# Performance work log

Measured on AMD Instinct MI355X. Metric: run time of the kernel, lower is better.

Reference implementation:

```python
import jax, jax.numpy as jnp
import numpy as np

B = 16          # number of point clouds (equal-sized, contiguous batch ids)
NC_PER = 1024   # coarse points per cloud
NF_PER = 4096   # fine points per cloud
K = 3           # knn_interpolate neighbors
C_IN = 512      # coarse feature channels
C_SKIP = 256    # skip feature channels
C_OUT = 512
BN_EPS = 1e-5


def setup_inputs() -> dict:
    key = jax.random.key(0)
    ks = jax.random.split(key, 8)
    Nc, Nf = B * NC_PER, B * NF_PER
    d_in = C_IN + C_SKIP
    x = jax.random.normal(ks[0], (Nc, C_IN), jnp.float32)
    pos = jax.random.uniform(ks[1], (Nc, 3), jnp.float32)
    batch = jnp.repeat(jnp.arange(B, dtype=jnp.int64), NC_PER)
    x_skip = jax.random.normal(ks[2], (Nf, C_SKIP), jnp.float32)
    pos_skip = jax.random.uniform(ks[3], (Nf, 3), jnp.float32)
    batch_skip = jnp.repeat(jnp.arange(B, dtype=jnp.int64), NF_PER)
    W1 = jax.random.normal(ks[4], (d_in, C_OUT), jnp.float32) / np.sqrt(d_in)
    W2 = jax.random.normal(ks[5], (C_OUT, C_OUT), jnp.float32) / np.sqrt(C_OUT)
    return {
        "x": x, "pos": pos, "batch": batch,
        "x_skip": x_skip, "pos_skip": pos_skip, "batch_skip": batch_skip,
        "W1": W1, "b1": jnp.zeros((C_OUT,), jnp.float32),
        "g1": jnp.ones((C_OUT,), jnp.float32), "be1": jnp.zeros((C_OUT,), jnp.float32),
        "W2": W2, "b2": jnp.zeros((C_OUT,), jnp.float32),
        "g2": jnp.ones((C_OUT,), jnp.float32), "be2": jnp.zeros((C_OUT,), jnp.float32),
    }


def _knn_interpolate(x, pos, pos_skip):
    # batches are contiguous and equal-sized -> reshape to [B, n, .] (honors batch/batch_skip)
    xb = x.reshape(B, NC_PER, C_IN)
    pc = pos.reshape(B, NC_PER, 3)
    pf = pos_skip.reshape(B, NF_PER, 3)
    # squared pairwise distances [B, NF_PER, NC_PER] via ||a||^2 + ||b||^2 - 2ab
    d2 = ((pf * pf).sum(-1)[:, :, None]
          + (pc * pc).sum(-1)[:, None, :]
          - 2.0 * jnp.einsum('bfd,bcd->bfc', pf, pc))
    neg_d2, idx = jax.lax.top_k(-d2, K)           # [B, NF_PER, K]
    w = 1.0 / jnp.maximum(-neg_d2, 1e-16)         # inverse squared-distance weights
    gathered = jax.vmap(lambda xi, ii: xi[ii])(xb, idx)   # [B, NF_PER, K, C_IN]
    y = (w[..., None] * gathered).sum(2) / w.sum(2)[..., None]
    return y.reshape(B * NF_PER, C_IN)


def _bn_act(h, g, be):
    # BatchNorm1d in training mode (biased variance) + ReLU
    mu = h.mean(0)
    var = ((h - mu) ** 2).mean(0)
    return jax.nn.relu((h - mu) * jax.lax.rsqrt(var + BN_EPS) * g + be)


def reference(x, pos, batch, x_skip, pos_skip, batch_skip,
              W1, b1, g1, be1, W2, b2, g2, be2):
    xi = _knn_interpolate(x, pos, pos_skip)        # [Nf, C_IN]
    h = jnp.concatenate([xi, x_skip], axis=1)      # [Nf, C_IN + C_SKIP]
    h = _bn_act(h @ W1 + b1, g1, be1)
    h = _bn_act(h @ W2 + b2, g2, be2)
    return (h, pos_skip, batch_skip)
```

## Files before the change

### kernel.cpp

```cpp
#include <hip/hip_runtime.h>
#include <cstdint>
#include <cstddef>

#define BATCHES   16
#define NC_PER    1024
#define NF_PER    4096
#define NC_TOT    (BATCHES * NC_PER)
#define NF_TOT    (BATCHES * NF_PER)
#define C_IN      512
#define C_SKIP    256
#define D_IN      (C_IN + C_SKIP)
#define C_OUT     512
#define BN_EPS    1e-5f

typedef __bf16 bf16x8 __attribute__((ext_vector_type(8)));
typedef __bf16 bf16x4 __attribute__((ext_vector_type(4)));
typedef float  f32x4  __attribute__((ext_vector_type(4)));

static_assert(sizeof(__bf16) == 2, "bf16 size");

__global__ __launch_bounds__(256) void transpose_to_bf16(
    const float* __restrict__ W, __bf16* __restrict__ Wt, int K, int N) {
  int idx = blockIdx.x * 256 + threadIdx.x;
  if (idx >= K * N) return;
  int n = idx / K;
  int k = idx - n * K;
  Wt[idx] = (__bf16)W[k * N + n];
}

__global__ __launch_bounds__(256) void knn_kernel(
    const float* __restrict__ pos,
    const float* __restrict__ pos_skip,
    int4*  __restrict__ idx3,
    float4* __restrict__ w3)
{
  __shared__ float s_pos[NC_PER * 3];
  __shared__ float s_pc2[NC_PER];
  __shared__ float s_pd[4][64][3];
  __shared__ int   s_pi[4][64][3];

  const int tid   = threadIdx.x;
  const int bi    = blockIdx.x;
  const int fbase = bi * 64;
  const int b     = fbase >> 12;
  const int cbase = b * NC_PER;

  for (int i = tid; i < NC_PER * 3; i += 256)
    s_pos[i] = pos[(size_t)cbase * 3 + i];
  __syncthreads();
  for (int j = tid; j < NC_PER; j += 256) {
    float cx = s_pos[j * 3 + 0], cy = s_pos[j * 3 + 1], cz = s_pos[j * 3 + 2];
    s_pc2[j] = __fadd_rn(__fadd_rn(__fmul_rn(cx, cx), __fmul_rn(cy, cy)),
                         __fmul_rn(cz, cz));
  }
  __syncthreads();

  const int p   = tid & 63;
  const int seg = tid >> 6;
  const int f   = fbase + p;
  const float px = pos_skip[f * 3 + 0];
  const float py = pos_skip[f * 3 + 1];
  const float pz = pos_skip[f * 3 + 2];
  const float pf2 = __fadd_rn(__fadd_rn(__fmul_rn(px, px), __fmul_rn(py, py)),
                              __fmul_rn(pz, pz));
  float b0 = 1e30f, b1 = 1e30f, b2 = 1e30f;
  int   i0 = 0,     i1 = 0,     i2 = 0;
  const int j0 = seg * 256;
#pragma unroll 4
  for (int jj = 0; jj < 256; ++jj) {
    const int j = j0 + jj;
    float cx = s_pos[j * 3 + 0], cy = s_pos[j * 3 + 1], cz = s_pos[j * 3 + 2];
    float dot = __fadd_rn(__fadd_rn(__fmul_rn(px, cx), __fmul_rn(py, cy)),
                          __fmul_rn(pz, cz));
    float d2 = __fsub_rn(__fadd_rn(pf2, s_pc2[j]), __fmul_rn(2.0f, dot));
    if (d2 < b2) {
      if (d2 < b1) {
        b2 = b1; i2 = i1;
        if (d2 < b0) { b1 = b0; i1 = i0; b0 = d2; i0 = j; }
        else         { b1 = d2; i1 = j; }
      } else { b2 = d2; i2 = j; }
    }
  }
  s_pd[seg][p][0] = b0; s_pd[seg][p][1] = b1; s_pd[seg][p][2] = b2;
  s_pi[seg][p][0] = i0; s_pi[seg][p][1] = i1; s_pi[seg][p][2] = i2;
  __syncthreads();

  if (tid < 64) {
    float m0 = 1e30f, m1 = 1e30f, m2 = 1e30f;
    int  mi0 = 0,    mi1 = 0,    mi2 = 0;
#pragma unroll
    for (int s = 0; s < 4; ++s)
#pragma unroll
      for (int k = 0; k < 3; ++k) {
        float d = s_pd[s][tid][k];
        int   i = s_pi[s][tid][k];
        if (d < m2 || (d == m2 && i < mi2)) {
          if (d < m1 || (d == m1 && i < mi1)) {
            m2 = m1; mi2 = mi1;
            if (d < m0 || (d == m0 && i < mi0)) {
              m1 = m0; mi1 = mi0; m0 = d; mi0 = i;
            } else { m1 = d; mi1 = i; }
          } else { m2 = d; mi2 = i; }
        }
      }
    float w0 = 1.0f / fmaxf(m0, 1e-16f);
    float w1 = 1.0f / fmaxf(m1, 1e-16f);
    float w2 = 1.0f / fmaxf(m2, 1e-16f);
    float inv = 1.0f / __fadd_rn(__fadd_rn(w0, w1), w2);
    const int fo = fbase + tid;
    idx3[fo] = make_int4(mi0, mi1, mi2, 0);
    w3[fo]   = make_float4(w0 * inv, w1 * inv, w2 * inv, 0.f);
  }
}

__global__ __launch_bounds__(256) void gather_interp(
    const float* __restrict__ x,
    const float* __restrict__ x_skip,
    const int4*  __restrict__ idx3,
    const float4* __restrict__ w3,
    __bf16* __restrict__ h0)
{
  const int bi   = blockIdx.x;
  const int xcd  = bi & 7;
  const int slot = bi >> 3;
  const int batch = xcd * 2 + (slot >> 10);
  const int blk   = slot & 1023;
  const int wv = threadIdx.x >> 6, ln = threadIdx.x & 63;
  const int f = batch * NF_PER + blk * 4 + wv;
  const int cbase = batch * NC_PER;

  const int4   id = idx3[f];
  const float4 w  = w3[f];
  const float* x0 = x + (size_t)(cbase + id.x) * C_IN;
  const float* x1 = x + (size_t)(cbase + id.y) * C_IN;
  const float* x2 = x + (size_t)(cbase + id.z) * C_IN;
  __bf16* o = h0 + (size_t)f * D_IN;
  const int c0 = ln * 4;
#pragma unroll
  for (int it = 0; it < 2; ++it) {
    const int c = c0 + it * 256;
    float4 a0 = *(const float4*)(x0 + c);
    float4 a1 = *(const float4*)(x1 + c);
    float4 a2 = *(const float4*)(x2 + c);
    bf16x4 ov;
    ov[0] = (__bf16)(w.x * a0.x + w.y * a1.x + w.z * a2.x);
    ov[1] = (__bf16)(w.x * a0.y + w.y * a1.y + w.z * a2.y);
    ov[2] = (__bf16)(w.x * a0.z + w.y * a1.z + w.z * a2.z);
    ov[3] = (__bf16)(w.x * a0.w + w.y * a1.w + w.z * a2.w);
    *(bf16x4*)(o + c) = ov;
  }
  float4 s = *(const float4*)(x_skip + (size_t)f * C_SKIP + c0);
  bf16x4 sv;
  sv[0] = (__bf16)s.x; sv[1] = (__bf16)s.y;
  sv[2] = (__bf16)s.z; sv[3] = (__bf16)s.w;
  *(bf16x4*)(o + C_IN + c0) = sv;
}

template <int K, bool BF16OUT>
__global__ __launch_bounds__(512, 2) void gemm_bt(
    const __bf16* __restrict__ A,
    const __bf16* __restrict__ Bt,
    const float*  __restrict__ bias,
    void* __restrict__ Cout,
    float* __restrict__ part1)
{
  constexpr int NT = K / 64;
  __shared__ __align__(16) __bf16 As[2 * 16384];
  __shared__ __align__(16) __bf16 Bs[2 * 16384];
  __shared__ float s_red[4][4][16][2];

  const int tid  = threadIdx.x;
  const int wave = tid >> 6, lane = tid & 63;
  const int quad = lane >> 4, l16 = lane & 15;
  const int wm = wave >> 2, wn = wave & 3;

  const int bid  = blockIdx.x;
  const int work = (bid & 7) * 64 + (bid >> 3);
  const int mt = work >> 1, nt = work & 1;
  const int m0 = mt * 256, n0 = nt * 256;

  const int rowA = wave * 8 + (lane >> 3);
  const int kOff = ((lane & 7) ^ (lane >> 3)) * 8;
  const int ldsChunkBase = (wave * 64) * 8;

  auto stage_half = [&](const __bf16* __restrict__ src, int rowBase, int t,
                        __bf16* dst) {
#pragma unroll
    for (int q = 0; q < 2; ++q) {
      __builtin_amdgcn_global_load_lds(
          (const __attribute__((address_space(1))) unsigned int*)(
              src + (size_t)(rowBase + q * 64 + rowA) * K + t * 64 + kOff),
          (__attribute__((address_space(3))) unsigned int*)(
              dst + q * 4096 + ldsChunkBase),
          16, 0, 0);
    }
  };

  f32x4 acc[8][4] = {};
  const int swz  = (l16 & 7) << 3;
  const int brow = (wn & 1) * 64;

  stage_half(A,  m0,       0, As);
  stage_half(Bt, n0,       0, Bs);
  stage_half(A,  m0 + 128, 0, As + 8192);
  stage_half(Bt, n0 + 128, 0, Bs + 8192);

  bf16x8 aA[4][2], bB[4][2];
#pragma unroll 2
  for (int t = 0; t < NT; ++t) {
    const int cur = t & 1;
    const __bf16* Ab = As + (cur * 2 + wm) * 8192;
    const __bf16* Bb = Bs + (cur * 2 + (wn >> 1)) * 8192;
    __bf16* Asn = As + (cur ^ 1) * 16384;
    __bf16* Bsn = Bs + (cur ^ 1) * 16384;

    if (t + 1 < NT) {
      stage_half(A,  m0,       t + 1, Asn);
      stage_half(Bt, n0,       t + 1, Bsn);
      asm volatile("s_waitcnt vmcnt(4)" ::: "memory");
    } else {
      asm volatile("s_waitcnt vmcnt(0)" ::: "memory");
    }
    __builtin_amdgcn_sched_barrier(0);
    __builtin_amdgcn_s_barrier();
#pragma unroll
    for (int mf = 0; mf < 4; ++mf)
#pragma unroll
      for (int ks = 0; ks < 2; ++ks)
        aA[mf][ks] = *(const bf16x8*)(Ab + (mf * 16 + l16) * 64 +
                                      ((ks * 32 + quad * 8) ^ swz));
#pragma unroll
    for (int nf = 0; nf < 2; ++nf)
#pragma unroll
      for (int ks = 0; ks < 2; ++ks)
        bB[nf][ks] = *(const bf16x8*)(Bb + (brow + nf * 16 + l16) * 64 +
                                      ((ks * 32 + quad * 8) ^ swz));
    __builtin_amdgcn_s_setprio(1);
#pragma unroll
    for (int mf = 0; mf < 4; ++mf)
#pragma unroll
      for (int nf = 0; nf < 2; ++nf)
#pragma unroll
        for (int ks = 0; ks < 2; ++ks)
          acc[mf][nf] = __builtin_amdgcn_mfma_f32_16x16x32_bf16(
              aA[mf][ks], bB[nf][ks], acc[mf][nf], 0, 0, 0);
    __builtin_amdgcn_s_setprio(0);
    __builtin_amdgcn_s_barrier();

    if (t + 1 < NT) {
      stage_half(A,  m0 + 128, t + 1, Asn + 8192);
      stage_half(Bt, n0 + 128, t + 1, Bsn + 8192);
    }
#pragma unroll
    for (int nf = 2; nf < 4; ++nf)
#pragma unroll
      for (int ks = 0; ks < 2; ++ks)
        bB[nf][ks] = *(const bf16x8*)(Bb + (brow + nf * 16 + l16) * 64 +
                                      ((ks * 32 + quad * 8) ^ swz));
    __builtin_amdgcn_s_setprio(1);
#pragma unroll
    for (int mf = 0; mf < 4; ++mf)
#pragma unroll
      for (int nf = 2; nf < 4; ++nf)
#pragma unroll
        for (int ks = 0; ks < 2; ++ks)
          acc[mf][nf] = __builtin_amdgcn_mfma_f32_16x16x32_bf16(
              aA[mf][ks], bB[nf][ks], acc[mf][nf], 0, 0, 0);
    __builtin_amdgcn_s_setprio(0);
    __builtin_amdgcn_s_barrier();

#pragma unroll
    for (int mf = 0; mf < 4; ++mf)
#pragma unroll
      for (int ks = 0; ks < 2; ++ks)
        aA[mf][ks] = *(const bf16x8*)(Ab + (64 + mf * 16 + l16) * 64 +
                                      ((ks * 32 + quad * 8) ^ swz));
    __builtin_amdgcn_s_setprio(1);
#pragma unroll
    for (int mf = 0; mf < 4; ++mf)
#pragma unroll
      for (int nf = 0; nf < 2; ++nf)
#pragma unroll
        for (int ks = 0; ks < 2; ++ks)
          acc[4 + mf][nf] = __builtin_amdgcn_mfma_f32_16x16x32_bf16(
              aA[mf][ks], bB[nf][ks], acc[4 + mf][nf], 0, 0, 0);
    __builtin_amdgcn_s_setprio(0);
    __builtin_amdgcn_s_barrier();

    __builtin_amdgcn_s_setprio(1);
#pragma unroll
    for (int mf = 0; mf < 4; ++mf)
#pragma unroll
      for (int nf = 2; nf < 4; ++nf)
#pragma unroll
        for (int ks = 0; ks < 2; ++ks)
          acc[4 + mf][nf] = __builtin_amdgcn_mfma_f32_16x16x32_bf16(
              aA[mf][ks], bB[nf][ks], acc[4 + mf][nf], 0, 0, 0);
    __builtin_amdgcn_s_setprio(0);
    __builtin_amdgcn_s_barrier();
  }

  float sArr[4], ssArr[4];
#pragma unroll
  for (int nf = 0; nf < 4; ++nf) {
    const int n = n0 + wn * 64 + nf * 16 + l16;
    const float bv = bias[n];
    float s = 0.f, ss = 0.f;
#pragma unroll
    for (int mf = 0; mf < 8; ++mf) {
      const int mb = m0 + wm * 128 + mf * 16 + quad * 4;
#pragma unroll
      for (int r = 0; r < 4; ++r) {
        const float v = acc[mf][nf][r] + bv;
        s += v; ss += v * v;
        if constexpr (BF16OUT)
          ((__bf16*)Cout)[(size_t)(mb + r) * 512 + n] = (__bf16)v;
        else
          ((float*)Cout)[(size_t)(mb + r) * 512 + n] = v;
      }
    }
    s  += __shfl_down(s, 32);  s  += __shfl_down(s, 16);
    ss += __shfl_down(ss, 32); ss += __shfl_down(ss, 16);
    sArr[nf] = s; ssArr[nf] = ss;
  }
  if (wm == 1 && quad == 0) {
#pragma unroll
    for (int nf = 0; nf < 4; ++nf) {
      s_red[wn][nf][l16][0] = sArr[nf];
      s_red[wn][nf][l16][1] = ssArr[nf];
    }
  }
  asm volatile("s_waitcnt lgkmcnt(0)" ::: "memory");
  __builtin_amdgcn_s_barrier();
  if (wm == 0 && quad == 0) {
    float* row = part1 + (size_t)mt * 1024;
#pragma unroll
    for (int nf = 0; nf < 4; ++nf) {
      const int n = n0 + wn * 64 + nf * 16 + l16;
      row[n]       = sArr[nf]  + s_red[wn][nf][l16][0];
      row[512 + n] = ssArr[nf] + s_red[wn][nf][l16][1];
    }
  }
}

__global__ __launch_bounds__(256) void reduce_partials(
    const float* __restrict__ part1, float* __restrict__ part2) {
  const int rb = blockIdx.x;
  const int t  = threadIdx.x;
#pragma unroll
  for (int k = 0; k < 4; ++k) {
    const int c = k * 256 + t;
    float acc = 0.f;
    const float* p = part1 + (size_t)rb * 16 * 1024 + c;
#pragma unroll
    for (int r = 0; r < 16; ++r) { acc += *p; p += 1024; }
    part2[rb * 1024 + c] = acc;
  }
}

__global__ void finalize_stats(const float* __restrict__ part2,
                               const float* __restrict__ g,
                               const float* __restrict__ be,
                               float* __restrict__ ab, float invM) {
  const int c = blockIdx.x * 256 + threadIdx.x;
  if (c < 512) {
    float s = 0.f, ss = 0.f;
#pragma unroll
    for (int r = 0; r < 16; ++r) {
      s  += part2[r * 1024 + c];
      ss += part2[r * 1024 + 512 + c];
    }
    float mean = s * invM;
    float var  = ss * invM - mean * mean;
    float a = g[c] * rsqrtf(var + BN_EPS);
    ab[c] = a;
    ab[512 + c] = be[c] - mean * a;
  }
}

__global__ __launch_bounds__(256) void bnrelu_bf16(
    __bf16* __restrict__ H, const float* __restrict__ ab) {
  const size_t e = ((size_t)blockIdx.x * 256 + threadIdx.x) * 4;
  const int c = (int)(e & 511);
  bf16x4* p = (bf16x4*)(H + e);
  bf16x4 h = *p;
#pragma unroll
  for (int i = 0; i < 4; ++i) {
    float v = (float)h[i];
    v = fmaxf(fmaf(v, ab[c + i], ab[512 + c + i]), 0.f);
    h[i] = (__bf16)v;
  }
  *p = h;
}

__global__ __launch_bounds__(256) void bnrelu_b2f(
    const __bf16* __restrict__ H, const float* __restrict__ ab,
    float* __restrict__ O) {
  const size_t e = ((size_t)blockIdx.x * 256 + threadIdx.x) * 4;
  const int c = (int)(e & 511);
  bf16x4 h = *(const bf16x4*)(H + e);
  float4 o;
  o.x = fmaxf(fmaf((float)h[0], ab[c + 0], ab[512 + c + 0]), 0.f);
  o.y = fmaxf(fmaf((float)h[1], ab[c + 1], ab[512 + c + 1]), 0.f);
  o.z = fmaxf(fmaf((float)h[2], ab[c + 2], ab[512 + c + 2]), 0.f);
  o.w = fmaxf(fmaf((float)h[3], ab[c + 3], ab[512 + c + 3]), 0.f);
  *(float4*)(O + e) = o;
}

__global__ __launch_bounds__(256) void tail_kernel(
    const float* __restrict__ pos_skip, float* __restrict__ out2) {
  const int i = blockIdx.x * 256 + threadIdx.x;
  if (i < NF_TOT * 3) {
    out2[i] = pos_skip[i];
  } else {
    const int f = i - NF_TOT * 3;
    out2[i] = (float)(f >> 12);
  }
}

extern "C" void kernel_launch(void* const* d_in, const int* in_sizes, int n_in,
                              void* d_out, int out_size, void* d_ws, size_t ws_size,
                              hipStream_t stream) {
  (void)in_sizes; (void)n_in; (void)out_size; (void)ws_size;

  const float* x        = (const float*)d_in[0];
  const float* pos      = (const float*)d_in[1];
  const float* x_skip   = (const float*)d_in[3];
  const float* pos_skip = (const float*)d_in[4];
  const float* W1  = (const float*)d_in[6];
  const float* b1  = (const float*)d_in[7];
  const float* g1  = (const float*)d_in[8];
  const float* be1 = (const float*)d_in[9];
  const float* W2  = (const float*)d_in[10];
  const float* b2  = (const float*)d_in[11];
  const float* g2  = (const float*)d_in[12];
  const float* be2 = (const float*)d_in[13];
  float* out = (float*)d_out;

  char* ws = (char*)d_ws;
  __bf16* h0   = (__bf16*)(ws);
  __bf16* h2   = (__bf16*)(ws);
  __bf16* h1   = (__bf16*)(ws + 100663296ull);
  __bf16* W1t  = (__bf16*)(ws + 167772160ull);
  __bf16* W2t  = (__bf16*)(ws + 168558592ull);
  float*  ab1   = (float*)(ws + 169086976ull);
  float*  ab2   = (float*)(ws + 169095168ull);
  int4*   idx3  = (int4*)(ws + 169099264ull);
  float4* w3    = (float4*)(ws + 170147840ull);
  float*  part1 = (float*)(ws + 169099264ull);
  float*  part2 = (float*)(ws + 171196416ull);

  transpose_to_bf16<<<(D_IN * C_OUT + 255) / 256, 256, 0, stream>>>(W1, W1t, D_IN, C_OUT);
  transpose_to_bf16<<<(C_OUT * C_OUT + 255) / 256, 256, 0, stream>>>(W2, W2t, C_OUT, C_OUT);

  knn_kernel<<<NF_TOT / 64, 256, 0, stream>>>(pos, pos_skip, idx3, w3);
  gather_interp<<<NF_TOT / 4, 256, 0, stream>>>(x, x_skip, idx3, w3, h0);

  gemm_bt<D_IN, true><<<512, 512, 0, stream>>>(h0, W1t, b1, (void*)h1, part1);
  reduce_partials<<<16, 256, 0, stream>>>(part1, part2);
  finalize_stats<<<2, 256, 0, stream>>>(part2, g1, be1, ab1, 1.0f / (float)NF_TOT);
  bnrelu_bf16<<<(NF_TOT * 512 / 4) / 256, 256, 0, stream>>>(h1, ab1);

  gemm_bt<C_OUT, true><<<512, 512, 0, stream>>>(h1, W2t, b2, (void*)h2, part1);
  reduce_partials<<<16, 256, 0, stream>>>(part1, part2);
  finalize_stats<<<2, 256, 0, stream>>>(part2, g2, be2, ab2, 1.0f / (float)NF_TOT);
  bnrelu_b2f<<<(NF_TOT * 512 / 4) / 256, 256, 0, stream>>>(h2, ab2, out);

  tail_kernel<<<(NF_TOT * 3 + NF_TOT + 255) / 256, 256, 0, stream>>>(
      pos_skip, out + (size_t)NF_TOT * 512);
}
```

Before: 506.4 us.

## Fuse BN1+ReLU into second GEMM A-load and stage GEMM output through LDS

Removes the standalone bnrelu_bf16 pass by loading GEMM2's A tiles into registers, applying the BN scale/shift and ReLU, and writing them to LDS inside the pipelined K-loop. The GEMM epilogue now stages bf16 outputs through LDS so that global stores are coalesced 16-byte rows instead of scattered 2-byte writes. It also merges the two weight transposes into one launch and widens bnrelu_b2f to 8 elements per thread. The trade-off is extra VALU work and a register round-trip for A inside GEMM2's main loop, plus more complex wait-count handling.

Result: faster. 472.0 us (-6.8%).

```diff
diff --git a/kernel.cpp b/kernel.cpp
--- a/kernel.cpp
+++ b/kernel.cpp
@@ -19,13 +19,26 @@
 
 static_assert(sizeof(__bf16) == 2, "bf16 size");
 
-__global__ __launch_bounds__(256) void transpose_to_bf16(
-    const float* __restrict__ W, __bf16* __restrict__ Wt, int K, int N) {
+__device__ __forceinline__ bf16x8 load16(const __bf16* p) {
+  f32x4 r;
+  asm volatile("global_load_dwordx4 %0, %1, off" : "=v"(r) : "v"(p));
+  union { f32x4 f; bf16x8 b; } u; u.f = r; return u.b;
+}
+
+__global__ __launch_bounds__(256) void transpose_both(
+    const float* __restrict__ W1, const float* __restrict__ W2,
+    __bf16* __restrict__ W1t, __bf16* __restrict__ W2t) {
   int idx = blockIdx.x * 256 + threadIdx.x;
-  if (idx >= K * N) return;
-  int n = idx / K;
-  int k = idx - n * K;
-  Wt[idx] = (__bf16)W[k * N + n];
+  if (idx < D_IN * C_OUT) {
+    int n = idx / D_IN, k = idx - n * D_IN;
+    W1t[idx] = (__bf16)W1[k * C_OUT + n];
+  } else {
+    idx -= D_IN * C_OUT;
+    if (idx < C_OUT * C_OUT) {
+      int n = idx >> 9, k = idx & 511;
+      W2t[idx] = (__bf16)W2[k * C_OUT + n];
+    }
+  }
 }
 
 __global__ __launch_bounds__(256) void knn_kernel(
@@ -156,18 +169,20 @@
   *(bf16x4*)(o + C_IN + c0) = sv;
 }
 
-template <int K, bool BF16OUT>
+template <int K, bool FUSE_BN>
 __global__ __launch_bounds__(512, 2) void gemm_bt(
     const __bf16* __restrict__ A,
     const __bf16* __restrict__ Bt,
     const float*  __restrict__ bias,
-    void* __restrict__ Cout,
-    float* __restrict__ part1)
+    __bf16* __restrict__ Cout,
+    float* __restrict__ part1,
+    const float* __restrict__ ab)
 {
   constexpr int NT = K / 64;
   __shared__ __align__(16) __bf16 As[2 * 16384];
   __shared__ __align__(16) __bf16 Bs[2 * 16384];
   __shared__ float s_red[4][4][16][2];
+  __shared__ float s_ab[1024];
 
   const int tid  = threadIdx.x;
   const int wave = tid >> 6, lane = tid & 63;
@@ -179,8 +194,9 @@
   const int mt = work >> 1, nt = work & 1;
   const int m0 = mt * 256, n0 = nt * 256;
 
-  const int rowA = wave * 8 + (lane >> 3);
-  const int kOff = ((lane & 7) ^ (lane >> 3)) * 8;
+  const int slot = lane & 7, rsub = lane >> 3;
+  const int rowA = wave * 8 + rsub;
+  const int kSw  = (slot ^ rsub) * 8;
   const int ldsChunkBase = (wave * 64) * 8;
 
   auto stage_half = [&](const __bf16* __restrict__ src, int rowBase, int t,
@@ -189,21 +205,65 @@
     for (int q = 0; q < 2; ++q) {
       __builtin_amdgcn_global_load_lds(
           (const __attribute__((address_space(1))) unsigned int*)(
-              src + (size_t)(rowBase + q * 64 + rowA) * K + t * 64 + kOff),
+              src + (size_t)(rowBase + q * 64 + rowA) * K + t * 64 + kSw),
           (__attribute__((address_space(3))) unsigned int*)(
               dst + q * 4096 + ldsChunkBase),
           16, 0, 0);
     }
   };
 
+  bf16x8 ar[4];
+
+  auto load_a_regs = [&](int tt) {
+#pragma unroll
+    for (int h = 0; h < 2; ++h)
+#pragma unroll
+      for (int q = 0; q < 2; ++q)
+        ar[h * 2 + q] = load16(A + (size_t)(m0 + h * 128 + q * 64 + rowA) * K +
+                               tt * 64 + slot * 8);
+  };
+  auto bn_write_A = [&](int tt, __bf16* dstbuf) {
+    const int cb = tt * 64 + slot * 8;
+    const float4 aL = *(const float4*)&s_ab[cb];
+    const float4 aH = *(const float4*)&s_ab[cb + 4];
+    const float4 bL = *(const float4*)&s_ab[512 + cb];
+    const float4 bH = *(const float4*)&s_ab[512 + cb + 4];
+#pragma unroll
+    for (int i = 0; i < 4; ++i) {
+      bf16x8 v = ar[i]; bf16x8 o;
+      o[0] = (__bf16)fmaxf(fmaf((float)v[0], aL.x, bL.x), 0.f);
+      o[1] = (__bf16)fmaxf(fmaf((float)v[1], aL.y, bL.y), 0.f);
+      o[2] = (__bf16)fmaxf(fmaf((float)v[2], aL.z, bL.z), 0.f);
+      o[3] = (__bf16)fmaxf(fmaf((float)v[3], aL.w, bL.w), 0.f);
+      o[4] = (__bf16)fmaxf(fmaf((float)v[4], aH.x, bH.x), 0.f);
+      o[5] = (__bf16)fmaxf(fmaf((float)v[5], aH.y, bH.y), 0.f);
+      o[6] = (__bf16)fmaxf(fmaf((float)v[6], aH.z, bH.z), 0.f);
+      o[7] = (__bf16)fmaxf(fmaf((float)v[7], aH.w, bH.w), 0.f);
+      const int h = i >> 1, q = i & 1;
+      *(bf16x8*)(dstbuf + h * 8192 + (size_t)(q * 64 + rowA) * 64 + kSw) = o;
+    }
+  };
+
   f32x4 acc[8][4] = {};
   const int swz  = (l16 & 7) << 3;
   const int brow = (wn & 1) * 64;
 
-  stage_half(A,  m0,       0, As);
-  stage_half(Bt, n0,       0, Bs);
-  stage_half(A,  m0 + 128, 0, As + 8192);
-  stage_half(Bt, n0 + 128, 0, Bs + 8192);
+  if constexpr (FUSE_BN) {
+    for (int i = tid; i < 1024; i += 512) s_ab[i] = ab[i];
+    load_a_regs(0);
+    stage_half(Bt, n0,       0, Bs);
+    stage_half(Bt, n0 + 128, 0, Bs + 8192);
+    __syncthreads();
+    bn_write_A(0, As);
+    asm volatile("s_waitcnt lgkmcnt(0)" ::: "memory");
+    __builtin_amdgcn_sched_barrier(0);
+    __builtin_amdgcn_s_barrier();
+  } else {
+    stage_half(A,  m0,       0, As);
+    stage_half(Bt, n0,       0, Bs);
+    stage_half(A,  m0 + 128, 0, As + 8192);
+    stage_half(Bt, n0 + 128, 0, Bs + 8192);
+  }
 
   bf16x8 aA[4][2], bB[4][2];
 #pragma unroll 2
@@ -215,9 +275,15 @@
     __bf16* Bsn = Bs + (cur ^ 1) * 16384;
 
     if (t + 1 < NT) {
-      stage_half(A,  m0,       t + 1, Asn);
-      stage_half(Bt, n0,       t + 1, Bsn);
-      asm volatile("s_waitcnt vmcnt(4)" ::: "memory");
+      if constexpr (FUSE_BN) {
+        load_a_regs(t + 1);
+        stage_half(Bt, n0, t + 1, Bsn);
+        asm volatile("s_waitcnt vmcnt(6)" ::: "memory");
+      } else {
+        stage_half(A,  m0, t + 1, Asn);
+        stage_half(Bt, n0, t + 1, Bsn);
+        asm volatile("s_waitcnt vmcnt(4)" ::: "memory");
+      }
     } else {
       asm volatile("s_waitcnt vmcnt(0)" ::: "memory");
     }
@@ -248,8 +314,9 @@
     __builtin_amdgcn_s_barrier();
 
     if (t + 1 < NT) {
-      stage_half(A,  m0 + 128, t + 1, Asn + 8192);
       stage_half(Bt, n0 + 128, t + 1, Bsn + 8192);
+      if constexpr (!FUSE_BN)
+        stage_half(A, m0 + 128, t + 1, Asn + 8192);
     }
 #pragma unroll
     for (int nf = 2; nf < 4; ++nf)
@@ -297,31 +364,40 @@
           acc[4 + mf][nf] = __builtin_amdgcn_mfma_f32_16x16x32_bf16(
               aA[mf][ks], bB[nf][ks], acc[4 + mf][nf], 0, 0, 0);
     __builtin_amdgcn_s_setprio(0);
+    if constexpr (FUSE_BN) {
+      if (t + 1 < NT) {
+        asm volatile("s_waitcnt vmcnt(4)" ::: "memory");
+        __builtin_amdgcn_sched_barrier(0);
+        bn_write_A(t + 1, Asn);
+        asm volatile("s_waitcnt lgkmcnt(0)" ::: "memory");
+        __builtin_amdgcn_sched_barrier(0);
+      }
+    }
     __builtin_amdgcn_s_barrier();
   }
 
   float sArr[4], ssArr[4];
-#pragma unroll
-  for (int nf = 0; nf < 4; ++nf) {
-    const int n = n0 + wn * 64 + nf * 16 + l16;
-    const float bv = bias[n];
-    float s = 0.f, ss = 0.f;
-#pragma unroll
-    for (int mf = 0; mf < 8; ++mf) {
-      const int mb = m0 + wm * 128 + mf * 16 + quad * 4;
-#pragma unroll
-      for (int r = 0; r < 4; ++r) {
-        const float v = acc[mf][nf][r] + bv;
-        s += v; ss += v * v;
-        if constexpr (BF16OUT)
-          ((__bf16*)Cout)[(size_t)(mb + r) * 512 + n] = (__bf16)v;
-        else
-          ((float*)Cout)[(size_t)(mb + r) * 512 + n] = v;
+  {
+    __bf16* cbase = wm ? Bs : As;
+#pragma unroll
+    for (int nf = 0; nf < 4; ++nf) {
+      const int cl = wn * 64 + nf * 16 + l16;
+      const float bv = bias[n0 + cl];
+      float s = 0.f, ss = 0.f;
+#pragma unroll
+      for (int mf = 0; mf < 8; ++mf) {
+        const int rl = (wm * 128 + mf * 16 + quad * 4) & 127;
+#pragma unroll
+        for (int r = 0; r < 4; ++r) {
+          const float v = acc[mf][nf][r] + bv;
+          s += v; ss += v * v;
+          cbase[(rl + r) * 256 + (cl ^ (quad << 4))] = (__bf16)v;
+        }
       }
-    }
-    s  += __shfl_down(s, 32);  s  += __shfl_down(s, 16);
-    ss += __shfl_down(ss, 32); ss += __shfl_down(ss, 16);
-    sArr[nf] = s; ssArr[nf] = ss;
+      s  += __shfl_down(s, 32);  s  += __shfl_down(s, 16);
+      ss += __shfl_down(ss, 32); ss += __shfl_down(ss, 16);
+      sArr[nf] = s; ssArr[nf] = ss;
+    }
   }
   if (wm == 1 && quad == 0) {
 #pragma unroll
@@ -330,15 +406,26 @@
       s_red[wn][nf][l16][1] = ssArr[nf];
     }
   }
-  asm volatile("s_waitcnt lgkmcnt(0)" ::: "memory");
-  __builtin_amdgcn_s_barrier();
+  __syncthreads();
+
+#pragma unroll
+  for (int p = 0; p < 16; ++p) {
+    const int i   = p * 512 + tid;
+    const int row = i >> 5;
+    const int cc  = (i & 31) * 8;
+    const __bf16* base = (p < 8) ? As : Bs;
+    bf16x8 v = *(const bf16x8*)&base[(row & 127) * 256 +
+                                     (cc ^ (((row >> 2) & 3) << 4))];
+    *(bf16x8*)&Cout[(size_t)(m0 + row) * 512 + n0 + cc] = v;
+  }
+
   if (wm == 0 && quad == 0) {
-    float* row = part1 + (size_t)mt * 1024;
+    float* rowp = part1 + (size_t)mt * 1024;
 #pragma unroll
     for (int nf = 0; nf < 4; ++nf) {
       const int n = n0 + wn * 64 + nf * 16 + l16;
-      row[n]       = sArr[nf]  + s_red[wn][nf][l16][0];
-      row[512 + n] = ssArr[nf] + s_red[wn][nf][l16][1];
+      rowp[n]       = sArr[nf]  + s_red[wn][nf][l16][0];
+      rowp[512 + n] = ssArr[nf] + s_red[wn][nf][l16][1];
     }
   }
 }
@@ -378,33 +465,23 @@
   }
 }
 
-__global__ __launch_bounds__(256) void bnrelu_bf16(
-    __bf16* __restrict__ H, const float* __restrict__ ab) {
-  const size_t e = ((size_t)blockIdx.x * 256 + threadIdx.x) * 4;
-  const int c = (int)(e & 511);
-  bf16x4* p = (bf16x4*)(H + e);
-  bf16x4 h = *p;
-#pragma unroll
-  for (int i = 0; i < 4; ++i) {
-    float v = (float)h[i];
-    v = fmaxf(fmaf(v, ab[c + i], ab[512 + c + i]), 0.f);
-    h[i] = (__bf16)v;
-  }
-  *p = h;
-}
-
 __global__ __launch_bounds__(256) void bnrelu_b2f(
     const __bf16* __restrict__ H, const float* __restrict__ ab,
     float* __restrict__ O) {
-  const size_t e = ((size_t)blockIdx.x * 256 + threadIdx.x) * 4;
+  const size_t e = ((size_t)blockIdx.x * 256 + threadIdx.x) * 8;
   const int c = (int)(e & 511);
-  bf16x4 h = *(const bf16x4*)(H + e);
-  float4 o;
-  o.x = fmaxf(fmaf((float)h[0], ab[c + 0], ab[512 + c + 0]), 0.f);
-  o.y = fmaxf(fmaf((float)h[1], ab[c + 1], ab[512 + c + 1]), 0.f);
-  o.z = fmaxf(fmaf((float)h[2], ab[c + 2], ab[512 + c + 2]), 0.f);
-  o.w = fmaxf(fmaf((float)h[3], ab[c + 3], ab[512 + c + 3]), 0.f);
-  *(float4*)(O + e) = o;
+  bf16x8 h = *(const bf16x8*)(H + e);
+  float4 o0, o1;
+  o0.x = fmaxf(fmaf((float)h[0], ab[c + 0], ab[512 + c + 0]), 0.f);
+  o0.y = fmaxf(fmaf((float)h[1], ab[c + 1], ab[512 + c + 1]), 0.f);
+  o0.z = fmaxf(fmaf((float)h[2], ab[c + 2], ab[512 + c + 2]), 0.f);
+  o0.w = fmaxf(fmaf((float)h[3], ab[c + 3], ab[512 + c + 3]), 0.f);
+  o1.x = fmaxf(fmaf((float)h[4], ab[c + 4], ab[512 + c + 4]), 0.f);
+  o1.y = fmaxf(fmaf((float)h[5], ab[c + 5], ab[512 + c + 5]), 0.f);
+  o1.z = fmaxf(fmaf((float)h[6], ab[c + 6], ab[512 + c + 6]), 0.f);
+  o1.w = fmaxf(fmaf((float)h[7], ab[c + 7], ab[512 + c + 7]), 0.f);
+  *(float4*)(O + e)     = o0;
+  *(float4*)(O + e + 4) = o1;
 }
 
 __global__ __launch_bounds__(256) void tail_kernel(
@@ -450,21 +527,20 @@
   float*  part1 = (float*)(ws + 169099264ull);
   float*  part2 = (float*)(ws + 171196416ull);
 
-  transpose_to_bf16<<<(D_IN * C_OUT + 255) / 256, 256, 0, stream>>>(W1, W1t, D_IN, C_OUT);
-  transpose_to_bf16<<<(C_OUT * C_OUT + 255) / 256, 256, 0, stream>>>(W2, W2t, C_OUT, C_OUT);
+  transpose_both<<<(D_IN * C_OUT + C_OUT * C_OUT + 255) / 256, 256, 0, stream>>>(
+      W1, W2, W1t, W2t);
 
   knn_kernel<<<NF_TOT / 64, 256, 0, stream>>>(pos, pos_skip, idx3, w3);
   gather_interp<<<NF_TOT / 4, 256, 0, stream>>>(x, x_skip, idx3, w3, h0);
 
-  gemm_bt<D_IN, true><<<512, 512, 0, stream>>>(h0, W1t, b1, (void*)h1, part1);
+  gemm_bt<D_IN, false><<<512, 512, 0, stream>>>(h0, W1t, b1, h1, part1, nullptr);
   reduce_partials<<<16, 256, 0, stream>>>(part1, part2);
   finalize_stats<<<2, 256, 0, stream>>>(part2, g1, be1, ab1, 1.0f / (float)NF_TOT);
-  bnrelu_bf16<<<(NF_TOT * 512 / 4) / 256, 256, 0, stream>>>(h1, ab1);
-
-  gemm_bt<C_OUT, true><<<512, 512, 0, stream>>>(h1, W2t, b2, (void*)h2, part1);
+
+  gemm_bt<C_OUT, true><<<512, 512, 0, stream>>>(h1, W2t, b2, h2, part1, ab1);
   reduce_partials<<<16, 256, 0, stream>>>(part1, part2);
   finalize_stats<<<2, 256, 0, stream>>>(part2, g2, be2, ab2, 1.0f / (float)NF_TOT);
-  bnrelu_b2f<<<(NF_TOT * 512 / 4) / 256, 256, 0, stream>>>(h2, ab2, out);
+  bnrelu_b2f<<<(NF_TOT * 512 / 8) / 256, 256, 0, stream>>>(h2, ab2, out);
 
   tail_kernel<<<(NF_TOT * 3 + NF_TOT + 255) / 256, 256, 0, stream>>>(
       pos_skip, out + (size_t)NF_TOT * 512);
```
